# Kernel optimization log

Measured on AMD Instinct MI355X. Metric: run time of the kernel, lower is better.

## Reference

```python
import jax, jax.numpy as jnp
import numpy as np

B, S, E, H = 64, 256, 512, 1024  # batch, seq_len, embed, hidden (dis_size=[512,1024,1024])


def _ln(x, g, b, eps=1e-5):
    # LayerNorm over last axis; x: [..., 3, H], g/b: [3, H] (per-gate affine)
    m = x.mean(-1, keepdims=True)
    v = ((x - m) ** 2).mean(-1, keepdims=True)
    return (x - m) * jax.lax.rsqrt(v + eps) * g + b


def _gru_cell(h, x, Wih, Whh, bih, bhh, gig, gib, ghg, ghb):
    Bsz = x.shape[0]
    Hh = h.shape[1]
    pi = _ln((x @ Wih.T + bih).reshape(Bsz, 3, Hh), gig, gib)
    ph = _ln((h @ Whh.T + bhh).reshape(Bsz, 3, Hh), ghg, ghb)
    r = jax.nn.sigmoid(pi[:, 0] + ph[:, 0])
    z = jax.nn.sigmoid(pi[:, 1] + ph[:, 1])
    n = jnp.tanh(pi[:, 2] + r * ph[:, 2])
    return (1.0 - z) * n + z * h


def _unroll(x, layers, W_out, b_out):
    # x: [B, S, E] -> scalar score per batch element from last hidden state
    xs = jnp.swapaxes(x, 0, 1)  # [S, B, E]
    for (Wih, Whh, bih, bhh, gig, gib, ghg, ghb) in layers:
        h0 = jnp.zeros((x.shape[0], Whh.shape[1]), x.dtype)

        def step(h, xt, Wih=Wih, Whh=Whh, bih=bih, bhh=bhh, gig=gig, gib=gib, ghg=ghg, ghb=ghb):
            h2 = _gru_cell(h, xt, Wih, Whh, bih, bhh, gig, gib, ghg, ghb)
            return h2, h2

        _, xs = jax.lax.scan(step, h0, xs)  # xs becomes [S, B, H]
    return (xs[-1] @ W_out.T + b_out)[:, 0]  # [B]


def setup_inputs() -> dict:
    key = jax.random.key(0)
    ks = jax.random.split(key, 12)
    sizes = [(E, H), (H, H)]  # (input_size, hidden_size) per layer
    inp = {
        "generated_data": jax.random.normal(ks[0], (B, S, E), jnp.float32),
        "true_data": jax.random.normal(ks[1], (B, S, E), jnp.float32),
    }
    for li, (ins, hs) in enumerate(sizes):
        k = jax.random.split(ks[2 + li], 4)
        inp[f"W_ih{li}"] = jax.random.normal(k[0], (3 * hs, ins), jnp.float32) * 0.02
        inp[f"W_hh{li}"] = jax.random.normal(k[1], (3 * hs, hs), jnp.float32) * 0.02
        inp[f"b_ih{li}"] = jnp.zeros((3 * hs,), jnp.float32)
        inp[f"b_hh{li}"] = jnp.zeros((3 * hs,), jnp.float32)
        inp[f"gi_g{li}"] = jnp.ones((3, hs), jnp.float32)
        inp[f"gi_b{li}"] = jnp.zeros((3, hs), jnp.float32)
        inp[f"gh_g{li}"] = jnp.ones((3, hs), jnp.float32)
        inp[f"gh_b{li}"] = jnp.zeros((3, hs), jnp.float32)
    inp["W_out"] = jax.random.normal(ks[10], (1, H), jnp.float32) * 0.02
    inp["b_out"] = jnp.zeros((1,), jnp.float32)
    return inp


def reference(generated_data, true_data,
              W_ih0, W_hh0, b_ih0, b_hh0, gi_g0, gi_b0, gh_g0, gh_b0,
              W_ih1, W_hh1, b_ih1, b_hh1, gi_g1, gi_b1, gh_g1, gh_b1,
              W_out, b_out):
    layers = [
        (W_ih0, W_hh0, b_ih0, b_hh0, gi_g0, gi_b0, gh_g0, gh_b0),
        (W_ih1, W_hh1, b_ih1, b_hh1, gi_g1, gi_b1, gh_g1, gh_b1),
    ]
    true_labels = _unroll(true_data, layers, W_out, b_out)
    gen_labels = _unroll(generated_data, layers, W_out, b_out)
    discriminator_loss = -true_labels.mean() + gen_labels.mean()
    generator_loss = -gen_labels.mean()
    return (discriminator_loss, generator_loss)
```

## Files before the change

kernel.cpp:

```cpp
#include <hip/hip_runtime.h>
#include <math.h>

#define NCH   128
#define SLEN  256
#define HDIM  1024
#define N3    3072

typedef __attribute__((ext_vector_type(8))) __bf16 bf16x8;
typedef __attribute__((ext_vector_type(4))) float  f32x4;

__device__ __forceinline__ f32x4 mfma_bf16(bf16x8 a, bf16x8 b, f32x4 c) {
  return __builtin_amdgcn_mfma_f32_16x16x32_bf16(a, b, c, 0, 0, 0);
}

__device__ __forceinline__ float ld_sc1_f32(const float* p) {
  return __hip_atomic_load(p, __ATOMIC_RELAXED, __HIP_MEMORY_SCOPE_AGENT);
}
__device__ __forceinline__ void st_sc1_f32(float* p, float v) {
  __hip_atomic_store(p, v, __ATOMIC_RELAXED, __HIP_MEMORY_SCOPE_AGENT);
}
__device__ __forceinline__ unsigned long long ld_sc1_u64(const unsigned long long* p) {
  return __hip_atomic_load(p, __ATOMIC_RELAXED, __HIP_MEMORY_SCOPE_AGENT);
}
__device__ __forceinline__ void st_sc1_u32(unsigned int* p, unsigned int v) {
  __hip_atomic_store(p, v, __ATOMIC_RELAXED, __HIP_MEMORY_SCOPE_AGENT);
}
__device__ __forceinline__ int ld_sc1_i32(const int* p) {
  return __hip_atomic_load(p, __ATOMIC_RELAXED, __HIP_MEMORY_SCOPE_AGENT);
}
__device__ __forceinline__ void st_sc1_i32(int* p, int v) {
  __hip_atomic_store(p, v, __ATOMIC_RELAXED, __HIP_MEMORY_SCOPE_AGENT);
}

__global__ void split_w(const float* __restrict__ src, __bf16* __restrict__ dh,
                        __bf16* __restrict__ dl, int n)
{
  int i = blockIdx.x * blockDim.x + threadIdx.x;
  if (i < n) {
    float x = src[i];
    __bf16 h = (__bf16)x;
    float r = x - (float)h;
    dh[i] = h;
    dl[i] = (__bf16)r;
  }
}

__global__ void zero_kernel(float* __restrict__ p, int n)
{
  int i = blockIdx.x * blockDim.x + threadIdx.x;
  if (i < n) p[i] = 0.f;
}

__global__ __launch_bounds__(256) void xproj_mfma(
    const float* __restrict__ A0, const float* __restrict__ A1,
    int chainsA0, int strideChain, int t0, int K, int lTc,
    const __bf16* __restrict__ Wh, const __bf16* __restrict__ Wl,
    const float* __restrict__ bias, float* __restrict__ out)
{
  __shared__ __bf16 Ah[4][128][8];
  __shared__ __bf16 Al[4][128][8];
  const int tid  = threadIdx.x;
  const int n0   = blockIdx.x * 64;
  const int row0 = blockIdx.y * 128;
  const int lane = tid & 63;
  const int wv   = tid >> 6;
  const int q    = lane >> 4;
  const int c15  = lane & 15;
  const int m_off = wv * 32;
  const int sr  = tid >> 1;
  const int sq0 = (tid & 1) * 2;
  const int sk  = (tid & 1) * 16;
  const int r     = row0 + sr;
  const int chain = r >> lTc;
  const int dt    = r & ((1 << lTc) - 1);
  const float* aptr = (chain < chainsA0)
      ? (A0 + ((size_t)chain * strideChain + t0 + dt) * K)
      : (A1 + ((size_t)(chain - chainsA0) * strideChain + t0 + dt) * K);

  f32x4 acc[2][4];
#pragma unroll
  for (int i = 0; i < 2; ++i)
#pragma unroll
    for (int j = 0; j < 4; ++j) acc[i][j] = (f32x4){0.f, 0.f, 0.f, 0.f};

  for (int k0 = 0; k0 < K; k0 += 32) {
    float f[16];
    *(float4*)(f + 0)  = *(const float4*)(aptr + k0 + sk + 0);
    *(float4*)(f + 4)  = *(const float4*)(aptr + k0 + sk + 4);
    *(float4*)(f + 8)  = *(const float4*)(aptr + k0 + sk + 8);
    *(float4*)(f + 12) = *(const float4*)(aptr + k0 + sk + 12);
    bf16x8 hv0, hv1, lv0, lv1;
#pragma unroll
    for (int e = 0; e < 8; ++e) {
      __bf16 h0 = (__bf16)f[e];
      hv0[e] = h0;  lv0[e] = (__bf16)(f[e] - (float)h0);
      __bf16 h1 = (__bf16)f[8 + e];
      hv1[e] = h1;  lv1[e] = (__bf16)(f[8 + e] - (float)h1);
    }
    __syncthreads();
    *(bf16x8*)&Ah[sq0][sr][0]     = hv0;
    *(bf16x8*)&Ah[sq0 + 1][sr][0] = hv1;
    *(bf16x8*)&Al[sq0][sr][0]     = lv0;
    *(bf16x8*)&Al[sq0 + 1][sr][0] = lv1;
    __syncthreads();

    bf16x8 a_h[2], a_l[2];
#pragma unroll
    for (int i = 0; i < 2; ++i) {
      a_h[i] = *(const bf16x8*)&Ah[q][m_off + i * 16 + c15][0];
      a_l[i] = *(const bf16x8*)&Al[q][m_off + i * 16 + c15][0];
    }
#pragma unroll
    for (int j = 0; j < 4; ++j) {
      const size_t woff = (size_t)(n0 + j * 16 + c15) * K + k0 + q * 8;
      bf16x8 b_h = *(const bf16x8*)(Wh + woff);
      bf16x8 b_l = *(const bf16x8*)(Wl + woff);
#pragma unroll
      for (int i = 0; i < 2; ++i) {
        acc[i][j] = mfma_bf16(a_h[i], b_h, acc[i][j]);
        acc[i][j] = mfma_bf16(a_h[i], b_l, acc[i][j]);
        acc[i][j] = mfma_bf16(a_l[i], b_h, acc[i][j]);
      }
    }
  }

#pragma unroll
  for (int j = 0; j < 4; ++j) {
    const int col = n0 + j * 16 + c15;
    const float bcol = bias[col];
#pragma unroll
    for (int i = 0; i < 2; ++i) {
#pragma unroll
      for (int rr = 0; rr < 4; ++rr) {
        const int m = m_off + i * 16 + q * 4 + rr;
        out[(size_t)(row0 + m) * N3 + col] = acc[i][j][rr] + bcol;
      }
    }
  }
}

__global__ __launch_bounds__(256) void ln_rows(float* __restrict__ a,
    const float* __restrict__ gw, const float* __restrict__ gb)
{
  const int row = blockIdx.x;
  const int tid = threadIdx.x;
  float* base = a + (size_t)row * N3;
  __shared__ float redS[4], redS2[4];
  __shared__ float s_mean, s_rstd;
  for (int g = 0; g < 3; ++g) {
    const int j = g * 1024 + tid * 4;
    float4 v = *(const float4*)(base + j);
    float s  = v.x + v.y + v.z + v.w;
    float s2 = v.x*v.x + v.y*v.y + v.z*v.z + v.w*v.w;
#pragma unroll
    for (int off = 32; off > 0; off >>= 1) {
      s  += __shfl_down(s, off);
      s2 += __shfl_down(s2, off);
    }
    if ((tid & 63) == 0) { redS[tid >> 6] = s; redS2[tid >> 6] = s2; }
    __syncthreads();
    if (tid == 0) {
      float S  = redS[0] + redS[1] + redS[2] + redS[3];
      float S2 = redS2[0] + redS2[1] + redS2[2] + redS2[3];
      float mean = S * (1.f / 1024.f);
      float var  = S2 * (1.f / 1024.f) - mean * mean;
      s_mean = mean;
      s_rstd = rsqrtf(var + 1e-5f);
    }
    __syncthreads();
    float mean = s_mean, rstd = s_rstd;
    float4 gwv = *(const float4*)(gw + j);
    float4 gbv = *(const float4*)(gb + j);
    float4 o;
    o.x = (v.x - mean) * rstd * gwv.x + gbv.x;
    o.y = (v.y - mean) * rstd * gwv.y + gbv.y;
    o.z = (v.z - mean) * rstd * gwv.z + gbv.z;
    o.w = (v.w - mean) * rstd * gwv.w + gbv.w;
    *(float4*)(base + j) = o;
    __syncthreads();
  }
}

__global__ __launch_bounds__(512, 2) void recur_pers(
    const __bf16* __restrict__ Wh, const __bf16* __restrict__ Wl,
    const float* __restrict__ bhh,
    const float* __restrict__ ghw, const float* __restrict__ ghb,
    const float* __restrict__ pi,
    unsigned int* __restrict__ Hpk,
    float* __restrict__ h_carry,
    float* __restrict__ hseq,
    float* __restrict__ stats_part,
    int* __restrict__ flag_a, int* __restrict__ flag_b,
    int Tc, int firstChunk)
{
  const int tid  = threadIdx.x;
  const int bid  = blockIdx.x;
  const int gid  = bid >> 5;
  const int ct   = bid & 31;
  const int lane = tid & 63;
  const int w    = tid >> 6;
  const int q    = lane >> 4;
  const int c15  = lane & 15;
  const int m    = tid & 15;
  const int col  = tid >> 4;
  const int ch   = gid * 16 + m;
  const int Hcol = ct * 32 + col;

  __shared__ float red[8 * 6 * 16 * 20];
  __shared__ float sred[8 * 16 * 6];
  __shared__ float sstat[96];

  bf16x8 bh[6][4], bl[6][4];
  const int kw = w * 128;
#pragma unroll
  for (int t = 0; t < 6; ++t) {
    const int gate = t >> 1, half = t & 1;
    const size_t nrow = (size_t)(gate * 1024 + ct * 32 + half * 16 + c15);
#pragma unroll
    for (int kc = 0; kc < 4; ++kc) {
      const size_t off = nrow * HDIM + kw + kc * 32 + q * 8;
      bh[t][kc] = *(const bf16x8*)(Wh + off);
      bl[t][kc] = *(const bf16x8*)(Wl + off);
    }
  }

  const float bias0 = bhh[Hcol], bias1 = bhh[1024 + Hcol], bias2 = bhh[2048 + Hcol];
  const float lw0 = ghw[Hcol], lw1 = ghw[1024 + Hcol], lw2 = ghw[2048 + Hcol];
  const float lb0 = ghb[Hcol], lb1 = ghb[1024 + Hcol], lb2 = ghb[2048 + Hcol];
  float hprev = firstChunk ? 0.f : h_carry[(size_t)ch * HDIM + Hcol];

  const size_t arowbase = (size_t)(gid * 16 + c15) * HDIM;
  float* my_part = stats_part + ((size_t)gid * 32 + ct) * 96;
  const int* fA = flag_a + (gid << 5);
  const int* fB = flag_b + (gid << 5);
  const int pidx = lane & 31;

  for (int dt = 0; dt < Tc; ++dt) {
    const float* pirow = pi + ((size_t)ch * Tc + dt) * N3 + Hcol;
    const float pr = pirow[0], pz = pirow[1024], pn = pirow[2048];

    if (w == 0 && dt > 0) {
      while (true) {
        int v = ld_sc1_i32(fB + pidx);
        if (!__any(v < dt)) break;
        __builtin_amdgcn_s_sleep(1);
      }
    }
    __syncthreads();
    __asm__ __volatile__("" ::: "memory");

    f32x4 acc[6];
#pragma unroll
    for (int t = 0; t < 6; ++t) acc[t] = (f32x4){0.f, 0.f, 0.f, 0.f};

    unsigned long long abuf[2][4];
#pragma unroll
    for (int j = 0; j < 4; ++j) {
      abuf[0][j] = ld_sc1_u64((const unsigned long long*)(Hpk + arowbase + kw + 0 * 32 + q * 8) + j);
      abuf[1][j] = ld_sc1_u64((const unsigned long long*)(Hpk + arowbase + kw + 1 * 32 + q * 8) + j);
    }
#pragma unroll
    for (int kc = 0; kc < 4; ++kc) {
      unsigned int u[8];
#pragma unroll
      for (int j = 0; j < 4; ++j) {
        u[2 * j]     = (unsigned int)(abuf[kc & 1][j]);
        u[2 * j + 1] = (unsigned int)(abuf[kc & 1][j] >> 32);
      }
      union { unsigned int d[4]; bf16x8 v; } uah, ual;
#pragma unroll
      for (int d = 0; d < 4; ++d) {
        uah.d[d] = __builtin_amdgcn_perm(u[2 * d + 1], u[2 * d], 0x05040100u);
        ual.d[d] = __builtin_amdgcn_perm(u[2 * d + 1], u[2 * d], 0x07060302u);
      }
      if (kc < 2) {
#pragma unroll
        for (int j = 0; j < 4; ++j)
          abuf[kc & 1][j] = ld_sc1_u64(
              (const unsigned long long*)(Hpk + arowbase + kw + (kc + 2) * 32 + q * 8) + j);
      }
      bf16x8 ah = uah.v, al = ual.v;
#pragma unroll
      for (int t = 0; t < 6; ++t) {
        acc[t] = mfma_bf16(ah, bh[t][kc], acc[t]);
        acc[t] = mfma_bf16(ah, bl[t][kc], acc[t]);
        acc[t] = mfma_bf16(al, bh[t][kc], acc[t]);
      }
    }

#pragma unroll
    for (int t = 0; t < 6; ++t) {
      const int idx = ((w * 6 + t) * 16 + c15) * 20 + q * 4;
      *(f32x4*)&red[idx] = acc[t];
    }
    __syncthreads();

    float phv0 = 0.f, phv1 = 0.f, phv2 = 0.f;
    {
      const int cn = col & 15;
      const int hi = col >> 4;
#pragma unroll
      for (int w8 = 0; w8 < 8; ++w8) {
        phv0 += red[((w8 * 6 + 0 * 2 + hi) * 16 + cn) * 20 + m];
        phv1 += red[((w8 * 6 + 1 * 2 + hi) * 16 + cn) * 20 + m];
        phv2 += red[((w8 * 6 + 2 * 2 + hi) * 16 + cn) * 20 + m];
      }
    }
    phv0 += bias0; phv1 += bias1; phv2 += bias2;

    {
      float s0 = phv0, s1 = phv1, s2 = phv2;
      float q0 = phv0 * phv0, q1 = phv1 * phv1, q2 = phv2 * phv2;
#pragma unroll
      for (int mm = 16; mm <= 32; mm <<= 1) {
        s0 += __shfl_xor(s0, mm); q0 += __shfl_xor(q0, mm);
        s1 += __shfl_xor(s1, mm); q1 += __shfl_xor(q1, mm);
        s2 += __shfl_xor(s2, mm); q2 += __shfl_xor(q2, mm);
      }
      if (lane < 16) {
        const int b = (w * 16 + lane) * 6;
        sred[b + 0] = s0; sred[b + 1] = q0;
        sred[b + 2] = s1; sred[b + 3] = q1;
        sred[b + 4] = s2; sred[b + 5] = q2;
      }
    }
    __syncthreads();

    if (tid < 96) {
      const int m6 = tid / 6;
      const int r6 = tid - m6 * 6;
      float v = 0.f;
#pragma unroll
      for (int w8 = 0; w8 < 8; ++w8) v += sred[(w8 * 16 + m6) * 6 + r6];
      st_sc1_f32(&my_part[tid], v);
    }
    __syncthreads();
    if (tid == 0) st_sc1_i32((int*)fA + ct, dt + 1);

    if (w == 0) {
      while (true) {
        int v = ld_sc1_i32(fA + pidx);
        if (!__any(v < dt + 1)) break;
        __builtin_amdgcn_s_sleep(1);
      }
    }
    __syncthreads();
    __asm__ __volatile__("" ::: "memory");

    {
      const int cidx = tid >> 4;
      const float* sp = stats_part + ((size_t)gid * 32 + cidx) * 96 + m * 6;
      float p0 = ld_sc1_f32(sp + 0), p1 = ld_sc1_f32(sp + 1), p2 = ld_sc1_f32(sp + 2);
      float p3 = ld_sc1_f32(sp + 3), p4 = ld_sc1_f32(sp + 4), p5 = ld_sc1_f32(sp + 5);
      p0 += __shfl_xor(p0, 16); p1 += __shfl_xor(p1, 16); p2 += __shfl_xor(p2, 16);
      p3 += __shfl_xor(p3, 16); p4 += __shfl_xor(p4, 16); p5 += __shfl_xor(p5, 16);
      p0 += __shfl_xor(p0, 32); p1 += __shfl_xor(p1, 32); p2 += __shfl_xor(p2, 32);
      p3 += __shfl_xor(p3, 32); p4 += __shfl_xor(p4, 32); p5 += __shfl_xor(p5, 32);
      if (lane < 16) {
        const int b = w * 104 + lane * 6;
        red[b + 0] = p0; red[b + 1] = p1; red[b + 2] = p2;
        red[b + 3] = p3; red[b + 4] = p4; red[b + 5] = p5;
      }
    }
    __syncthreads();
    if (tid < 96) {
      float v = 0.f;
#pragma unroll
      for (int w8 = 0; w8 < 8; ++w8) v += red[w8 * 104 + tid];
      sstat[tid] = v;
    }
    __syncthreads();

    {
      const int b = m * 6;
      const float mean0 = sstat[b + 0] * (1.f / 1024.f);
      const float var0  = sstat[b + 1] * (1.f / 1024.f) - mean0 * mean0;
      const float mean1 = sstat[b + 2] * (1.f / 1024.f);
      const float var1  = sstat[b + 3] * (1.f / 1024.f) - mean1 * mean1;
      const float mean2 = sstat[b + 4] * (1.f / 1024.f);
      const float var2  = sstat[b + 5] * (1.f / 1024.f) - mean2 * mean2;
      const float nh0 = (phv0 - mean0) * rsqrtf(var0 + 1e-5f) * lw0 + lb0;
      const float nh1 = (phv1 - mean1) * rsqrtf(var1 + 1e-5f) * lw1 + lb1;
      const float nh2 = (phv2 - mean2) * rsqrtf(var2 + 1e-5f) * lw2 + lb2;
      const float r  = 1.f / (1.f + expf(-(pr + nh0)));
      const float z  = 1.f / (1.f + expf(-(pz + nh1)));
      const float nn = tanhf(pn + r * nh2);
      const float hn = (1.f - z) * nn + z * hprev;
      hprev = hn;
      const __bf16 hb = (__bf16)hn;
      const __bf16 lo = (__bf16)(hn - (float)hb);
      unsigned short hs, ls;
      __builtin_memcpy(&hs, &hb, 2);
      __builtin_memcpy(&ls, &lo, 2);
      st_sc1_u32(Hpk + (size_t)ch * HDIM + Hcol,
                 (unsigned int)hs | ((unsigned int)ls << 16));
      if (hseq) hseq[((size_t)ch * Tc + dt) * HDIM + Hcol] = hn;
      if (dt == Tc - 1) h_carry[(size_t)ch * HDIM + Hcol] = hn;
    }
    __syncthreads();
    if (tid == 0) st_sc1_i32((int*)fB + ct, dt + 1);
  }
}

__global__ __launch_bounds__(256) void label_kernel(const float* __restrict__ h,
    const float* __restrict__ Wout, const float* __restrict__ bout,
    float* __restrict__ labels)
{
  const int c = blockIdx.x;
  const int tid = threadIdx.x;
  __shared__ float red[4];
  float4 hv = *(const float4*)(h + (size_t)c * HDIM + tid * 4);
  float4 wv = *(const float4*)(Wout + tid * 4);
  float s = hv.x * wv.x + hv.y * wv.y + hv.z * wv.z + hv.w * wv.w;
#pragma unroll
  for (int off = 32; off > 0; off >>= 1) s += __shfl_down(s, off);
  if ((tid & 63) == 0) red[tid >> 6] = s;
  __syncthreads();
  if (tid == 0) labels[c] = red[0] + red[1] + red[2] + red[3] + bout[0];
}

__global__ void loss_kernel(const float* __restrict__ labels, float* __restrict__ out)
{
  const int tid = threadIdx.x;
  __shared__ float rg[2], rt[2];
  float v = labels[tid];
  float g = (tid < 64) ? v : 0.f;
  float t = (tid >= 64) ? v : 0.f;
#pragma unroll
  for (int off = 32; off > 0; off >>= 1) {
    g += __shfl_down(g, off);
    t += __shfl_down(t, off);
  }
  if ((tid & 63) == 0) { rg[tid >> 6] = g; rt[tid >> 6] = t; }
  __syncthreads();
  if (tid == 0) {
    float gm = (rg[0] + rg[1]) * (1.f / 64.f);
    float tm = (rt[0] + rt[1]) * (1.f / 64.f);
    out[0] = -tm + gm;
    out[1] = -gm;
  }
}

extern "C" void kernel_launch(void* const* d_in, const int* in_sizes, int n_in,
                              void* d_out, int out_size, void* d_ws, size_t ws_size,
                              hipStream_t stream)
{
  const float* gen  = (const float*)d_in[0];
  const float* tru  = (const float*)d_in[1];
  const float* Wih0 = (const float*)d_in[2];
  const float* Whh0 = (const float*)d_in[3];
  const float* bih0 = (const float*)d_in[4];
  const float* bhh0 = (const float*)d_in[5];
  const float* gig0 = (const float*)d_in[6];
  const float* gib0 = (const float*)d_in[7];
  const float* ghg0 = (const float*)d_in[8];
  const float* ghb0 = (const float*)d_in[9];
  const float* Wih1 = (const float*)d_in[10];
  const float* Whh1 = (const float*)d_in[11];
  const float* bih1 = (const float*)d_in[12];
  const float* bhh1 = (const float*)d_in[13];
  const float* gig1 = (const float*)d_in[14];
  const float* gib1 = (const float*)d_in[15];
  const float* ghg1 = (const float*)d_in[16];
  const float* ghb1 = (const float*)d_in[17];
  const float* Wout = (const float*)d_in[18];
  const float* bout = (const float*)d_in[19];
  float* out = (float*)d_out;

  __bf16* bp = (__bf16*)d_ws;
  __bf16* Whh0h = bp;  bp += (size_t)N3 * HDIM;
  __bf16* Whh0l = bp;  bp += (size_t)N3 * HDIM;
  __bf16* Whh1h = bp;  bp += (size_t)N3 * HDIM;
  __bf16* Whh1l = bp;  bp += (size_t)N3 * HDIM;
  __bf16* Wih1h = bp;  bp += (size_t)N3 * HDIM;
  __bf16* Wih1l = bp;  bp += (size_t)N3 * HDIM;
  __bf16* Wih0h = bp;  bp += (size_t)N3 * 512;
  __bf16* Wih0l = bp;  bp += (size_t)N3 * 512;
  unsigned int* H0pk = (unsigned int*)bp;
  unsigned int* H1pk = H0pk + (size_t)NCH * HDIM;
  const size_t bf16Bytes = ((char*)(H1pk + (size_t)NCH * HDIM)) - (char*)d_ws;

  const size_t fixedF = 2 * (size_t)NCH * HDIM + 256 + 8 * 32 * 96 + 1024;
  int Tc = 256;
  while (Tc > 1) {
    size_t needF = (size_t)NCH * Tc * (N3 + HDIM) + fixedF;
    if (bf16Bytes + needF * 4 <= ws_size) break;
    Tc >>= 1;
  }
  int lTc = 0;
  while ((1 << lTc) < Tc) ++lTc;

  float* fp       = (float*)((char*)d_ws + bf16Bytes);
  float* pi_chunk = fp;   fp += (size_t)NCH * Tc * N3;
  float* h0_chunk = fp;   fp += (size_t)NCH * Tc * HDIM;
  float* h_cur0   = fp;   fp += (size_t)NCH * HDIM;
  float* h_cur1   = fp;   fp += (size_t)NCH * HDIM;
  float* labels   = fp;   fp += 256;
  float* stats    = fp;   fp += 8 * 32 * 96;
  int*   flag_a   = (int*)fp;
  int*   flag_b   = flag_a + 256;

  {
    const int nW = N3 * HDIM;
    split_w<<<(nW + 255) / 256, 256, 0, stream>>>(Whh0, Whh0h, Whh0l, nW);
    split_w<<<(nW + 255) / 256, 256, 0, stream>>>(Whh1, Whh1h, Whh1l, nW);
    split_w<<<(nW + 255) / 256, 256, 0, stream>>>(Wih1, Wih1h, Wih1l, nW);
    const int nW0 = N3 * 512;
    split_w<<<(nW0 + 255) / 256, 256, 0, stream>>>(Wih0, Wih0h, Wih0l, nW0);
  }
  zero_kernel<<<(2 * NCH * HDIM) / 256, 256, 0, stream>>>((float*)H0pk, 2 * NCH * HDIM);

  const int nChunks = SLEN / Tc;
  for (int cidx = 0; cidx < nChunks; ++cidx) {
    const int t0 = cidx * Tc;
    const int first = (cidx == 0) ? 1 : 0;
    xproj_mfma<<<dim3(48, Tc), 256, 0, stream>>>(
        gen, tru, 64, SLEN, t0, 512, lTc, Wih0h, Wih0l, bih0, pi_chunk);
    ln_rows<<<NCH * Tc, 256, 0, stream>>>(pi_chunk, gig0, gib0);
    zero_kernel<<<2, 256, 0, stream>>>((float*)flag_a, 512);
    {
      const __bf16* a0 = Whh0h; const __bf16* a1 = Whh0l;
      const float* a2 = bhh0; const float* a3 = ghg0; const float* a4 = ghb0;
      const float* a5 = pi_chunk; unsigned int* a6 = H0pk; float* a7 = h_cur0;
      float* a8 = h0_chunk; float* a9 = stats; int* a10 = flag_a; int* a11 = flag_b;
      int a12 = Tc; int a13 = first;
      void* args[] = {&a0,&a1,&a2,&a3,&a4,&a5,&a6,&a7,&a8,&a9,&a10,&a11,&a12,&a13};
      hipLaunchCooperativeKernel((void*)recur_pers, dim3(256), dim3(512),
                                 args, 0, stream);
    }
    xproj_mfma<<<dim3(48, Tc), 256, 0, stream>>>(
        h0_chunk, h0_chunk, NCH, Tc, 0, 1024, lTc, Wih1h, Wih1l, bih1, pi_chunk);
    ln_rows<<<NCH * Tc, 256, 0, stream>>>(pi_chunk, gig1, gib1);
    zero_kernel<<<2, 256, 0, stream>>>((float*)flag_a, 512);
    {
      const __bf16* a0 = Whh1h; const __bf16* a1 = Whh1l;
      const float* a2 = bhh1; const float* a3 = ghg1; const float* a4 = ghb1;
      const float* a5 = pi_chunk; unsigned int* a6 = H1pk; float* a7 = h_cur1;
      float* a8 = nullptr; float* a9 = stats; int* a10 = flag_a; int* a11 = flag_b;
      int a12 = Tc; int a13 = first;
      void* args[] = {&a0,&a1,&a2,&a3,&a4,&a5,&a6,&a7,&a8,&a9,&a10,&a11,&a12,&a13};
      hipLaunchCooperativeKernel((void*)recur_pers, dim3(256), dim3(512),
                                 args, 0, stream);
    }
  }

  label_kernel<<<NCH, 256, 0, stream>>>(h_cur1, Wout, bout, labels);
  loss_kernel<<<1, 128, 0, stream>>>(labels, out);
}
```

Baseline: 9.547 ms.

## Widen xproj N-tile, split LayerNorm per gate, launch recurrence without cooperative API

The input-projection GEMM now covers 128 output columns per block instead of 64, halving the grid and reusing each staged A tile across twice as many MFMAs, at the cost of more accumulator registers. LayerNorm is split so each block normalizes one gate segment (3x grid), which removes two in-loop barriers per row and adds parallelism. The persistent recurrence kernel is launched with a plain launch instead of hipLaunchCooperativeKernel to cut launch overhead. This relies on all 256 blocks being co-resident for the flag-based grid sync, which is no longer guaranteed.

```diff
diff --git a/kernel.cpp b/kernel.cpp
--- a/kernel.cpp
+++ b/kernel.cpp
@@ -60,7 +60,7 @@
   __shared__ __bf16 Ah[4][128][8];
   __shared__ __bf16 Al[4][128][8];
   const int tid  = threadIdx.x;
-  const int n0   = blockIdx.x * 64;
+  const int n0   = blockIdx.x * 128;
   const int row0 = blockIdx.y * 128;
   const int lane = tid & 63;
   const int wv   = tid >> 6;
@@ -77,11 +77,11 @@
       ? (A0 + ((size_t)chain * strideChain + t0 + dt) * K)
       : (A1 + ((size_t)(chain - chainsA0) * strideChain + t0 + dt) * K);
 
-  f32x4 acc[2][4];
+  f32x4 acc[2][8];
 #pragma unroll
   for (int i = 0; i < 2; ++i)
 #pragma unroll
-    for (int j = 0; j < 4; ++j) acc[i][j] = (f32x4){0.f, 0.f, 0.f, 0.f};
+    for (int j = 0; j < 8; ++j) acc[i][j] = (f32x4){0.f, 0.f, 0.f, 0.f};
 
   for (int k0 = 0; k0 < K; k0 += 32) {
     float f[16];
@@ -111,7 +111,7 @@
       a_l[i] = *(const bf16x8*)&Al[q][m_off + i * 16 + c15][0];
     }
 #pragma unroll
-    for (int j = 0; j < 4; ++j) {
+    for (int j = 0; j < 8; ++j) {
       const size_t woff = (size_t)(n0 + j * 16 + c15) * K + k0 + q * 8;
       bf16x8 b_h = *(const bf16x8*)(Wh + woff);
       bf16x8 b_l = *(const bf16x8*)(Wl + woff);
@@ -125,7 +125,7 @@
   }
 
 #pragma unroll
-  for (int j = 0; j < 4; ++j) {
+  for (int j = 0; j < 8; ++j) {
     const int col = n0 + j * 16 + c15;
     const float bcol = bias[col];
 #pragma unroll
@@ -143,42 +143,40 @@
     const float* __restrict__ gw, const float* __restrict__ gb)
 {
   const int row = blockIdx.x;
+  const int g   = blockIdx.y;
   const int tid = threadIdx.x;
-  float* base = a + (size_t)row * N3;
+  float* base = a + (size_t)row * N3 + g * 1024;
   __shared__ float redS[4], redS2[4];
   __shared__ float s_mean, s_rstd;
-  for (int g = 0; g < 3; ++g) {
-    const int j = g * 1024 + tid * 4;
-    float4 v = *(const float4*)(base + j);
-    float s  = v.x + v.y + v.z + v.w;
-    float s2 = v.x*v.x + v.y*v.y + v.z*v.z + v.w*v.w;
-#pragma unroll
-    for (int off = 32; off > 0; off >>= 1) {
-      s  += __shfl_down(s, off);
-      s2 += __shfl_down(s2, off);
-    }
-    if ((tid & 63) == 0) { redS[tid >> 6] = s; redS2[tid >> 6] = s2; }
-    __syncthreads();
-    if (tid == 0) {
-      float S  = redS[0] + redS[1] + redS[2] + redS[3];
-      float S2 = redS2[0] + redS2[1] + redS2[2] + redS2[3];
-      float mean = S * (1.f / 1024.f);
-      float var  = S2 * (1.f / 1024.f) - mean * mean;
-      s_mean = mean;
-      s_rstd = rsqrtf(var + 1e-5f);
-    }
-    __syncthreads();
-    float mean = s_mean, rstd = s_rstd;
-    float4 gwv = *(const float4*)(gw + j);
-    float4 gbv = *(const float4*)(gb + j);
-    float4 o;
-    o.x = (v.x - mean) * rstd * gwv.x + gbv.x;
-    o.y = (v.y - mean) * rstd * gwv.y + gbv.y;
-    o.z = (v.z - mean) * rstd * gwv.z + gbv.z;
-    o.w = (v.w - mean) * rstd * gwv.w + gbv.w;
-    *(float4*)(base + j) = o;
-    __syncthreads();
-  }
+  const int j = tid * 4;
+  float4 v = *(const float4*)(base + j);
+  float s  = v.x + v.y + v.z + v.w;
+  float s2 = v.x*v.x + v.y*v.y + v.z*v.z + v.w*v.w;
+#pragma unroll
+  for (int off = 32; off > 0; off >>= 1) {
+    s  += __shfl_down(s, off);
+    s2 += __shfl_down(s2, off);
+  }
+  if ((tid & 63) == 0) { redS[tid >> 6] = s; redS2[tid >> 6] = s2; }
+  __syncthreads();
+  if (tid == 0) {
+    float S  = redS[0] + redS[1] + redS[2] + redS[3];
+    float S2 = redS2[0] + redS2[1] + redS2[2] + redS2[3];
+    float mean = S * (1.f / 1024.f);
+    float var  = S2 * (1.f / 1024.f) - mean * mean;
+    s_mean = mean;
+    s_rstd = rsqrtf(var + 1e-5f);
+  }
+  __syncthreads();
+  float mean = s_mean, rstd = s_rstd;
+  float4 gwv = *(const float4*)(gw + g * 1024 + j);
+  float4 gbv = *(const float4*)(gb + g * 1024 + j);
+  float4 o;
+  o.x = (v.x - mean) * rstd * gwv.x + gbv.x;
+  o.y = (v.y - mean) * rstd * gwv.y + gbv.y;
+  o.z = (v.z - mean) * rstd * gwv.z + gbv.z;
+  o.w = (v.w - mean) * rstd * gwv.w + gbv.w;
+  *(float4*)(base + j) = o;
 }
 
 __global__ __launch_bounds__(512, 2) void recur_pers(
@@ -514,34 +512,20 @@
   for (int cidx = 0; cidx < nChunks; ++cidx) {
     const int t0 = cidx * Tc;
     const int first = (cidx == 0) ? 1 : 0;
-    xproj_mfma<<<dim3(48, Tc), 256, 0, stream>>>(
+    xproj_mfma<<<dim3(24, Tc), 256, 0, stream>>>(
         gen, tru, 64, SLEN, t0, 512, lTc, Wih0h, Wih0l, bih0, pi_chunk);
-    ln_rows<<<NCH * Tc, 256, 0, stream>>>(pi_chunk, gig0, gib0);
+    ln_rows<<<dim3(NCH * Tc, 3), 256, 0, stream>>>(pi_chunk, gig0, gib0);
     zero_kernel<<<2, 256, 0, stream>>>((float*)flag_a, 512);
-    {
-      const __bf16* a0 = Whh0h; const __bf16* a1 = Whh0l;
-      const float* a2 = bhh0; const float* a3 = ghg0; const float* a4 = ghb0;
-      const float* a5 = pi_chunk; unsigned int* a6 = H0pk; float* a7 = h_cur0;
-      float* a8 = h0_chunk; float* a9 = stats; int* a10 = flag_a; int* a11 = flag_b;
-      int a12 = Tc; int a13 = first;
-      void* args[] = {&a0,&a1,&a2,&a3,&a4,&a5,&a6,&a7,&a8,&a9,&a10,&a11,&a12,&a13};
-      hipLaunchCooperativeKernel((void*)recur_pers, dim3(256), dim3(512),
-                                 args, 0, stream);
-    }
-    xproj_mfma<<<dim3(48, Tc), 256, 0, stream>>>(
+    recur_pers<<<256, 512, 0, stream>>>(
+        Whh0h, Whh0l, bhh0, ghg0, ghb0, pi_chunk, H0pk, h_cur0,
+        h0_chunk, stats, flag_a, flag_b, Tc, first);
+    xproj_mfma<<<dim3(24, Tc), 256, 0, stream>>>(
         h0_chunk, h0_chunk, NCH, Tc, 0, 1024, lTc, Wih1h, Wih1l, bih1, pi_chunk);
-    ln_rows<<<NCH * Tc, 256, 0, stream>>>(pi_chunk, gig1, gib1);
+    ln_rows<<<dim3(NCH * Tc, 3), 256, 0, stream>>>(pi_chunk, gig1, gib1);
     zero_kernel<<<2, 256, 0, stream>>>((float*)flag_a, 512);
-    {
-      const __bf16* a0 = Whh1h; const __bf16* a1 = Whh1l;
-      const float* a2 = bhh1; const float* a3 = ghg1; const float* a4 = ghb1;
-      const float* a5 = pi_chunk; unsigned int* a6 = H1pk; float* a7 = h_cur1;
-      float* a8 = nullptr; float* a9 = stats; int* a10 = flag_a; int* a11 = flag_b;
-      int a12 = Tc; int a13 = first;
-      void* args[] = {&a0,&a1,&a2,&a3,&a4,&a5,&a6,&a7,&a8,&a9,&a10,&a11,&a12,&a13};
-      hipLaunchCooperativeKernel((void*)recur_pers, dim3(256), dim3(512),
-                                 args, 0, stream);
-    }
+    recur_pers<<<256, 512, 0, stream>>>(
+        Whh1h, Whh1l, bhh1, ghg1, ghb1, pi_chunk, H1pk, h_cur1,
+        (float*)nullptr, stats, flag_a, flag_b, Tc, first);
   }
 
   label_kernel<<<NCH, 256, 0, stream>>>(h_cur1, Wout, bout, labels);
```

Measured after the change: 9.400 ms (median of 2 runs). No clear change (-1.5%).
